# Performance work log

Hardware: AMD Instinct MI355X
Metric: run time of the kernel (lower is better)

## Reference

```python
import jax, jax.numpy as jnp
import numpy as np
from jax import lax

BN_EPS = 1e-5


def _conv(x, w):
    # stride-1, VALID conv; the torch 'locally connected' layer shares weights
    # across pixels, so it is exactly a standard conv2d.
    return lax.conv_general_dilated(
        x, w, window_strides=(1, 1), padding='VALID',
        dimension_numbers=('NCHW', 'OIHW', 'NCHW'))


def _batchnorm(x, gamma, beta):
    # training-mode BatchNorm2d: batch statistics over (N, H, W)
    mean = jnp.mean(x, axis=(0, 2, 3), keepdims=True)
    var = jnp.var(x, axis=(0, 2, 3), keepdims=True)
    xhat = (x - mean) * lax.rsqrt(var + BN_EPS)
    return xhat * gamma[None, :, None, None] + beta[None, :, None, None]


def setup_inputs() -> dict:
    key = jax.random.key(0)
    ks = jax.random.split(key, 6)
    B = 16384
    x = jax.random.normal(ks[0], (B, 256), dtype=jnp.float32)
    w1 = jax.random.normal(ks[1], (16, 1, 3, 3), dtype=jnp.float32)
    w2 = jax.random.normal(ks[2], (32, 16, 2, 2), dtype=jnp.float32)
    w3 = jax.random.normal(ks[3], (64, 32, 1, 1), dtype=jnp.float32)
    fan_in = 64 * 13 * 13
    bound = 1.0 / np.sqrt(fan_in)
    fc_w = jax.random.uniform(ks[4], (10, fan_in), minval=-bound, maxval=bound, dtype=jnp.float32)
    fc_b = jax.random.uniform(ks[5], (10,), minval=-bound, maxval=bound, dtype=jnp.float32)
    return {
        'x': x, 'w1': w1, 'w2': w2, 'w3': w3,
        'g1': jnp.ones((16,), jnp.float32), 'b1': jnp.zeros((16,), jnp.float32),
        'g2': jnp.ones((32,), jnp.float32), 'b2': jnp.zeros((32,), jnp.float32),
        'g3': jnp.ones((64,), jnp.float32), 'b3': jnp.zeros((64,), jnp.float32),
        'fc_w': fc_w, 'fc_b': fc_b,
    }


def reference(x, w1, w2, w3, g1, b1, g2, b2, g3, b3, fc_w, fc_b):
    h = x.reshape(-1, 1, 16, 16)                     # [B,1,16,16]
    h = jax.nn.relu(_batchnorm(_conv(h, w1), g1, b1))  # [B,16,14,14]
    h = jax.nn.relu(_batchnorm(_conv(h, w2), g2, b2))  # [B,32,13,13]
    h = jax.nn.relu(_batchnorm(_conv(h, w3), g3, b3))  # [B,64,13,13]
    h = h.reshape(h.shape[0], -1)                    # [B, 64*13*13]
    # dropout is identity in eval/deterministic mode
    return h @ fc_w.T + fc_b                         # [B,10]
```

## Files before the change

### kernel.cpp

```cpp
#include <hip/hip_runtime.h>


#define NPART 1024
#define P2_OFF 32768
#define ST_OFF 229376
#define ST1 ST_OFF
#define ST2 (ST_OFF + 32)
#define ST3 (ST_OFF + 96)
#define C2R_OFF 230400
#define C1R_OFF 231424
#define C2P_OFF 262144
#define A2G_BYTE 5242880ull
#define FCB_N (13 * 8192)
#define A1S 24
#define A1B 384
#define A3P 1048

typedef __attribute__((ext_vector_type(8))) short bf16x8;
typedef __attribute__((ext_vector_type(4))) float f32x4;
typedef __attribute__((ext_vector_type(4))) unsigned int u32x4;

__device__ __forceinline__ unsigned int f2bf(float f) {
  unsigned int u = __float_as_uint(f);
  return (u + 0x7fffu + ((u >> 16) & 1u)) >> 16;
}
__device__ __forceinline__ unsigned int pkbf(float a, float b) {
  unsigned ua = __float_as_uint(a) + 0x8000u;
  unsigned ub = __float_as_uint(b) + 0x8000u;
  return __builtin_amdgcn_perm(ub, ua, 0x07060302u);
}
__device__ __forceinline__ short cvtbf(float a) {
  return (short)((__float_as_uint(a) + 0x8000u) >> 16);
}
__device__ __forceinline__ bf16x8 mkfrag(uint2 a, uint2 b) {
  u32x4 u = {a.x, a.y, b.x, b.y};
  return __builtin_bit_cast(bf16x8, u);
}

__device__ __forceinline__ void conv1_mfma(
    const float* __restrict__ sxi,
    short* ph_buf,
    int r, int b, int q, bf16x8 a1f, f32x4 c1i)
{
  bf16x8 bf = {0, 0, 0, 0, 0, 0, 0, 0};
  unsigned* bu = (unsigned*)&bf;
  if (q == 0) {
    bu[0] = pkbf(sxi[r * 16 + b],           sxi[r * 16 + b + 1]);
    bu[1] = pkbf(sxi[r * 16 + b + 2],       sxi[(r + 1) * 16 + b]);
    bu[2] = pkbf(sxi[(r + 1) * 16 + b + 1], sxi[(r + 1) * 16 + b + 2]);
    bu[3] = pkbf(sxi[(r + 2) * 16 + b],     sxi[(r + 2) * 16 + b + 1]);
  } else if (q == 1) {
    bu[0] = pkbf(sxi[(r + 2) * 16 + b + 2], 0.f);
  }
  f32x4 acc = c1i;
  acc = __builtin_amdgcn_mfma_f32_16x16x32_bf16(a1f, bf, acc, 0, 0, 0);
  float v0 = acc[0] > 0.f ? acc[0] : 0.f;
  float v1 = acc[1] > 0.f ? acc[1] : 0.f;
  float v2 = acc[2] > 0.f ? acc[2] : 0.f;
  float v3 = acc[3] > 0.f ? acc[3] : 0.f;
  uint2 pk;
  pk.x = pkbf(v0, v1);
  pk.y = pkbf(v2, v3);
  *(uint2*)(ph_buf + (r & 1) * A1B + b * A1S + 4 * q) = pk;
}

__device__ __forceinline__ bf16x8 conv1_afrag(const float* w1, float rs1b,
                                              int b, int q) {
  bf16x8 v;
#pragma unroll
  for (int j = 0; j < 8; ++j) {
    int tap = 8 * q + j;
    v[j] = (tap < 9) ? (short)f2bf(w1[b * 9 + tap] * rs1b) : (short)0;
  }
  return v;
}

__global__ __launch_bounds__(256) void k1_xsyrk(
    const float* __restrict__ x, float* __restrict__ parts)
{
  __shared__ float sx[16 * 256];
  const int tid = threadIdx.x, w = tid >> 6, lane = tid & 63;
  const int b = lane & 15, q = lane >> 4;
  {
    const float4* xs = (const float4*)(x + (size_t)blockIdx.x * (16 * 256));
    float4* sd = (float4*)sx;
    for (int e = tid; e < 16 * 64; e += 256) sd[e] = xs[e];
  }
  __syncthreads();
  const int di = (b < 9) ? (b / 3) : 0;
  const int dj = (b < 9) ? (b - di * 3) : 0;
  const int h = q >> 1, jb = (q & 1) * 8;
  f32x4 acc = {0.f, 0.f, 0.f, 0.f};
#pragma unroll 1
  for (int t = 0; t < 4; ++t) {
    const float* sxi = sx + (w * 4 + t) * 256;
#pragma unroll 1
    for (int s = 0; s < 7; ++s) {
      bf16x8 af;
      unsigned* au = (unsigned*)&af;
      if (b < 9) {
        const float* srow = sxi + (2 * s + h + di) * 16 + dj;
#pragma unroll
        for (int cc = 0; cc < 4; ++cc) {
          float v0 = (jb + 2 * cc     < 14) ? srow[jb + 2 * cc]     : 0.f;
          float v1 = (jb + 2 * cc + 1 < 14) ? srow[jb + 2 * cc + 1] : 0.f;
          au[cc] = pkbf(v0, v1);
        }
      } else if (b == 9) {
#pragma unroll
        for (int cc = 0; cc < 4; ++cc) {
          unsigned lo = (jb + 2 * cc     < 14) ? 0x3F80u : 0u;
          unsigned hi = (jb + 2 * cc + 1 < 14) ? 0x3F800000u : 0u;
          au[cc] = lo | hi;
        }
      } else {
#pragma unroll
        for (int cc = 0; cc < 4; ++cc) au[cc] = 0u;
      }
      acc = __builtin_amdgcn_mfma_f32_16x16x32_bf16(af, af, acc, 0, 0, 0);
    }
  }
  __syncthreads();
  float* redc = sx;
#pragma unroll
  for (int rr = 0; rr < 4; ++rr)
    redc[w * 256 + (4 * q + rr) * 16 + b] = acc[rr];
  __syncthreads();
  parts[blockIdx.x * 256 + tid] =
      redc[tid] + redc[256 + tid] + redc[512 + tid] + redc[768 + tid];
}

__global__ __launch_bounds__(256) void k_stats1a(
    const float* __restrict__ parts, float* __restrict__ ws)
{
  const int e = blockIdx.x, tid = threadIdx.x;
  const int w = tid >> 6, lane = tid & 63;
  __shared__ float rs[4];
  float s = 0.f;
#pragma unroll 4
  for (int i = tid; i < 1024; i += 256) s += parts[i * 256 + e];
#pragma unroll
  for (int d = 1; d < 64; d <<= 1) s += __shfl_xor(s, d);
  if (lane == 0) rs[w] = s;
  __syncthreads();
  if (tid == 0) ws[C1R_OFF + e] = rs[0] + rs[1] + rs[2] + rs[3];
}

__global__ __launch_bounds__(64) void k_stats1b(
    const float* __restrict__ w1, const float* __restrict__ gamma,
    const float* __restrict__ beta, float* __restrict__ ws)
{
  const int c = threadIdx.x;
  if (c >= 16) return;
  const float* C = ws + C1R_OFF;
  float wr[9];
#pragma unroll
  for (int p = 0; p < 9; ++p) wr[p] = w1[c * 9 + p];
  float msum = 0.f;
#pragma unroll
  for (int p = 0; p < 9; ++p) msum += wr[p] * C[9 * 16 + p];
  float e2 = 0.f;
#pragma unroll
  for (int a = 0; a < 9; ++a)
#pragma unroll
    for (int bb = 0; bb < 9; ++bb)
      e2 += wr[a] * wr[bb] * C[a * 16 + bb];
  const float inv_n = 1.0f / (16384.0f * 196.0f);
  float mean = msum * inv_n;
  float var  = e2 * inv_n - mean * mean;
  float sv   = gamma[c] * rsqrtf(var + 1e-5f);
  ws[ST1 + c]      = sv;
  ws[ST1 + 16 + c] = beta[c] - mean * sv;
}

__global__ __launch_bounds__(256) void k_stats2(
    const float* __restrict__ gamma, const float* __restrict__ beta,
    float* __restrict__ ws, int nch, int part_off, int st_off, float inv_n)
{
  const int c = blockIdx.x, tid = threadIdx.x;
  const int w = tid >> 6, lane = tid & 63;
  __shared__ float rs[4], rq[4];
  float s = 0.f, q = 0.f;
#pragma unroll 4
  for (int i = tid; i < NPART; i += 256) {
    s += ws[part_off + i * 2 * nch + c];
    q += ws[part_off + i * 2 * nch + nch + c];
  }
#pragma unroll
  for (int d = 1; d < 64; d <<= 1) {
    s += __shfl_xor(s, d);
    q += __shfl_xor(q, d);
  }
  if (lane == 0) { rs[w] = s; rq[w] = q; }
  __syncthreads();
  if (tid == 0) {
    float st = rs[0] + rs[1] + rs[2] + rs[3];
    float qt = rq[0] + rq[1] + rq[2] + rq[3];
    float mean = st * inv_n;
    float var  = qt * inv_n - mean * mean;
    float sv   = gamma[c] * rsqrtf(var + 1e-5f);
    ws[st_off + c]       = sv;
    ws[st_off + nch + c] = beta[c] - mean * sv;
  }
}

__global__ __launch_bounds__(256) void k3_conv2_stats(
    const float* __restrict__ x, const float* __restrict__ w1,
    const float* __restrict__ w2, float* __restrict__ ws)
{
  __shared__ float sx_s[16 * 256 + 16];
  __shared__ alignas(16) short a1h[4 * 2 * A1B];
  __shared__ float redf[256];
  const int tid = threadIdx.x, w = tid >> 6, lane = tid & 63;
  const int b = lane & 15, q = lane >> 4;
  {
    const float4* xs = (const float4*)(x + (size_t)blockIdx.x * (16 * 256));
    float4* sd = (float4*)sx_s;
    for (int e = tid; e < 16 * 64; e += 256) sd[e] = xs[e];
    if (tid < 16) sx_s[16 * 256 + tid] = 0.f;
  }
  bf16x8 a1f = conv1_afrag(w1, ws[ST1 + b], b, q);
  f32x4 c1i;
#pragma unroll
  for (int r = 0; r < 4; ++r) c1i[r] = ws[ST1 + 16 + 4 * q + r];
  bf16x8 b2h[4];
#pragma unroll
  for (int ks = 0; ks < 2; ++ks)
#pragma unroll
    for (int nt = 0; nt < 2; ++nt) {
      bf16x8 vh;
#pragma unroll
      for (int j = 0; j < 8; ++j) {
        int kk = 8 * (q & 1) + j, dj = q >> 1;
        vh[j] = (short)f2bf(w2[(nt * 16 + b) * 64 + kk * 4 + ks * 2 + dj]);
      }
      b2h[ks * 2 + nt] = vh;
    }
  const float vb = (b < 13) ? 1.f : 0.f;
  const int colAr = (b + (q >> 1) < 15) ? (b + (q >> 1)) : 15;
  const int offAl = colAr * A1S + 8 * (q & 1);
  __syncthreads();

  float s2r[2][4] = {{0.f,0.f,0.f,0.f},{0.f,0.f,0.f,0.f}};
  float q2r[2][4] = {{0.f,0.f,0.f,0.f},{0.f,0.f,0.f,0.f}};
  short* ph = a1h + w * (2 * A1B);
#pragma unroll 1
  for (int t = 0; t < 4; ++t) {
    const float* sxi = sx_s + (w * 4 + t) * 256;
    conv1_mfma(sxi, ph, 0, b, q, a1f, c1i);
    __builtin_amdgcn_wave_barrier();
#pragma unroll 1
    for (int i = 0; i < 13; ++i) {
      conv1_mfma(sxi, ph, i + 1, b, q, a1f, c1i);
      __builtin_amdgcn_wave_barrier();
      bf16x8 ah0 = *(const bf16x8*)(ph + (i & 1) * A1B + offAl);
      bf16x8 ah1 = *(const bf16x8*)(ph + ((i + 1) & 1) * A1B + offAl);
      f32x4 acc2[2] = {{0.f,0.f,0.f,0.f},{0.f,0.f,0.f,0.f}};
#pragma unroll
      for (int nt = 0; nt < 2; ++nt) {
        acc2[nt] = __builtin_amdgcn_mfma_f32_16x16x32_bf16(b2h[nt], ah0, acc2[nt], 0, 0, 0);
        acc2[nt] = __builtin_amdgcn_mfma_f32_16x16x32_bf16(b2h[2 + nt], ah1, acc2[nt], 0, 0, 0);
      }
#pragma unroll
      for (int nt = 0; nt < 2; ++nt)
#pragma unroll
        for (int r = 0; r < 4; ++r) {
          float ym = acc2[nt][r] * vb;
          s2r[nt][r] += ym;
          q2r[nt][r] = fmaf(ym, acc2[nt][r], q2r[nt][r]);
        }
      __builtin_amdgcn_wave_barrier();
    }
  }
#pragma unroll
  for (int nt = 0; nt < 2; ++nt)
#pragma unroll
    for (int r = 0; r < 4; ++r) {
      float sv = s2r[nt][r], qv = q2r[nt][r];
      sv += __shfl_xor(sv, 1); sv += __shfl_xor(sv, 2);
      sv += __shfl_xor(sv, 4); sv += __shfl_xor(sv, 8);
      qv += __shfl_xor(qv, 1); qv += __shfl_xor(qv, 2);
      qv += __shfl_xor(qv, 4); qv += __shfl_xor(qv, 8);
      if (b == 0) {
        redf[w * 64 + nt * 16 + 4 * q + r]      = sv;
        redf[w * 64 + 32 + nt * 16 + 4 * q + r] = qv;
      }
    }
  __syncthreads();
  if (tid < 64)
    ws[P2_OFF + blockIdx.x * 64 + tid] =
        redf[tid] + redf[64 + tid] + redf[128 + tid] + redf[192 + tid];
}

__global__ __launch_bounds__(256) void k5_a2(
    const float* __restrict__ x, const float* __restrict__ w1,
    const float* __restrict__ w2, float* __restrict__ ws,
    short* __restrict__ a2g, float* __restrict__ parts)
{
  __shared__ float sx_s[16 * 256 + 16];
  __shared__ alignas(16) short a1h[4 * 2 * A1B];
  __shared__ float s2red[4 * 32];
  const int tid = threadIdx.x, w = tid >> 6, lane = tid & 63;
  const int b = lane & 15, q = lane >> 4;
  {
    const float4* xs = (const float4*)(x + (size_t)blockIdx.x * (16 * 256));
    float4* sd = (float4*)sx_s;
    for (int e = tid; e < 16 * 64; e += 256) sd[e] = xs[e];
    if (tid < 16) sx_s[16 * 256 + tid] = 0.f;
  }
  bf16x8 a1f = conv1_afrag(w1, ws[ST1 + b], b, q);
  f32x4 c1i;
#pragma unroll
  for (int r = 0; r < 4; ++r) c1i[r] = ws[ST1 + 16 + 4 * q + r];
  bf16x8 b2h[4];
#pragma unroll
  for (int ks = 0; ks < 2; ++ks)
#pragma unroll
    for (int nt = 0; nt < 2; ++nt) {
      float rs2b = ws[ST2 + nt * 16 + b];
      bf16x8 vh;
#pragma unroll
      for (int j = 0; j < 8; ++j) {
        int kk = 8 * (q & 1) + j, dj = q >> 1;
        vh[j] = (short)f2bf(w2[(nt * 16 + b) * 64 + kk * 4 + ks * 2 + dj] * rs2b);
      }
      b2h[ks * 2 + nt] = vh;
    }
  f32x4 c2i[2];
#pragma unroll
  for (int nt = 0; nt < 2; ++nt) {
    float t2b = ws[ST2 + 32 + nt * 16 + b];
#pragma unroll
    for (int r = 0; r < 4; ++r)
      c2i[nt][r] = (4 * q + r < 13) ? t2b : -1e30f;
  }
  const int colAr = (b + (q >> 1) < 15) ? (b + (q >> 1)) : 15;
  const int offAl = colAr * A1S + 8 * (q & 1);
  const u32x4 ou = {0x3F803F80u, 0x3F803F80u, 0x3F803F80u, 0x3F803F80u};
  const bf16x8 ones = __builtin_bit_cast(bf16x8, ou);
  __syncthreads();

  f32x4 accT0 = {0.f,0.f,0.f,0.f}, accT1 = {0.f,0.f,0.f,0.f},
        accT2 = {0.f,0.f,0.f,0.f};
  f32x4 accS0 = {0.f,0.f,0.f,0.f}, accS1 = {0.f,0.f,0.f,0.f};
  short* ph = a1h + w * (2 * A1B);
#pragma unroll 1
  for (int t = 0; t < 4; ++t) {
    const int img = blockIdx.x * 16 + w * 4 + t;
    const float* sxi = sx_s + (w * 4 + t) * 256;
    short* p0 = a2g + (size_t)img * 5408 + (size_t)(4 * q) * 32 + b;
    conv1_mfma(sxi, ph, 0, b, q, a1f, c1i);
    __builtin_amdgcn_wave_barrier();
    uint2 pkp[2];
#pragma unroll 1
    for (int i = 0; i < 13; ++i) {
      conv1_mfma(sxi, ph, i + 1, b, q, a1f, c1i);
      __builtin_amdgcn_wave_barrier();
      bf16x8 ah0 = *(const bf16x8*)(ph + (i & 1) * A1B + offAl);
      bf16x8 ah1 = *(const bf16x8*)(ph + ((i + 1) & 1) * A1B + offAl);
      uint2 pkc[2];
#pragma unroll
      for (int nt = 0; nt < 2; ++nt) {
        f32x4 acc2 = c2i[nt];
        acc2 = __builtin_amdgcn_mfma_f32_16x16x32_bf16(ah0, b2h[nt], acc2, 0, 0, 0);
        acc2 = __builtin_amdgcn_mfma_f32_16x16x32_bf16(ah1, b2h[2 + nt], acc2, 0, 0, 0);
        float v0 = acc2[0] > 0.f ? acc2[0] : 0.f;
        float v1 = acc2[1] > 0.f ? acc2[1] : 0.f;
        float v2 = acc2[2] > 0.f ? acc2[2] : 0.f;
        float v3 = acc2[3] > 0.f ? acc2[3] : 0.f;
        uint2 pk;
        pk.x = pkbf(v0, v1);
        pk.y = pkbf(v2, v3);
        short* pp = p0 + nt * 16;
        pp[0] = (short)pk.x;
        if (q < 3) {
          pp[32] = (short)(pk.x >> 16);
          pp[64] = (short)pk.y;
          pp[96] = (short)(pk.y >> 16);
        }
        pkc[nt] = pk;
      }
      p0 += 416;
      if (i & 1) {
        bf16x8 xf0 = mkfrag(pkp[0], pkc[0]);
        bf16x8 xf1 = mkfrag(pkp[1], pkc[1]);
        accT0 = __builtin_amdgcn_mfma_f32_16x16x32_bf16(xf0, xf0, accT0, 0, 0, 0);
        accT1 = __builtin_amdgcn_mfma_f32_16x16x32_bf16(xf0, xf1, accT1, 0, 0, 0);
        accT2 = __builtin_amdgcn_mfma_f32_16x16x32_bf16(xf1, xf1, accT2, 0, 0, 0);
        accS0 = __builtin_amdgcn_mfma_f32_16x16x32_bf16(ones, xf0, accS0, 0, 0, 0);
        accS1 = __builtin_amdgcn_mfma_f32_16x16x32_bf16(ones, xf1, accS1, 0, 0, 0);
      } else {
        pkp[0] = pkc[0];
        pkp[1] = pkc[1];
      }
      __builtin_amdgcn_wave_barrier();
    }
    {
      uint2 zz; zz.x = 0u; zz.y = 0u;
      bf16x8 xf0 = mkfrag(pkp[0], zz);
      bf16x8 xf1 = mkfrag(pkp[1], zz);
      accT0 = __builtin_amdgcn_mfma_f32_16x16x32_bf16(xf0, xf0, accT0, 0, 0, 0);
      accT1 = __builtin_amdgcn_mfma_f32_16x16x32_bf16(xf0, xf1, accT1, 0, 0, 0);
      accT2 = __builtin_amdgcn_mfma_f32_16x16x32_bf16(xf1, xf1, accT2, 0, 0, 0);
      accS0 = __builtin_amdgcn_mfma_f32_16x16x32_bf16(ones, xf0, accS0, 0, 0, 0);
      accS1 = __builtin_amdgcn_mfma_f32_16x16x32_bf16(ones, xf1, accS1, 0, 0, 0);
    }
  }
  if (q == 0) {
    s2red[w * 32 + b]      = accS0[0];
    s2red[w * 32 + 16 + b] = accS1[0];
  }
  float* redc = sx_s;
#pragma unroll
  for (int rr = 0; rr < 4; ++rr) {
    int m = 4 * q + rr;
    redc[w * 1024 + 0   + m * 16 + b] = accT0[rr];
    redc[w * 1024 + 256 + m * 16 + b] = accT1[rr];
    redc[w * 1024 + 512 + m * 16 + b] = accT2[rr];
  }
  __syncthreads();
  for (int e = tid; e < 768; e += 256)
    parts[blockIdx.x * 800 + e] =
        redc[e] + redc[1024 + e] + redc[2048 + e] + redc[3072 + e];
  if (tid < 32)
    parts[blockIdx.x * 800 + 768 + tid] =
        s2red[tid] + s2red[32 + tid] + s2red[64 + tid] + s2red[96 + tid];
}

__global__ __launch_bounds__(256) void k_statsC(
    const float* __restrict__ parts, float* __restrict__ ws)
{
  const int e = blockIdx.x, tid = threadIdx.x;
  const int w = tid >> 6, lane = tid & 63;
  __shared__ float rs[4];
  float s = 0.f;
#pragma unroll 4
  for (int i = tid; i < 1024; i += 256) s += parts[i * 800 + e];
#pragma unroll
  for (int d = 1; d < 64; d <<= 1) s += __shfl_xor(s, d);
  if (lane == 0) rs[w] = s;
  __syncthreads();
  if (tid == 0) ws[C2R_OFF + e] = rs[0] + rs[1] + rs[2] + rs[3];
}

__global__ __launch_bounds__(64) void k_stats3n(
    const float* __restrict__ w3, const float* __restrict__ gamma,
    const float* __restrict__ beta, float* __restrict__ ws)
{
  const int c3 = threadIdx.x;
  if (c3 >= 64) return;
  const float* C2R = ws + C2R_OFF;
  float wr[32];
#pragma unroll
  for (int k = 0; k < 32; ++k) wr[k] = w3[c3 * 32 + k];
  const float inv_n = 1.0f / (16384.0f * 169.0f);
  float msum = 0.f;
#pragma unroll
  for (int k = 0; k < 32; ++k) msum += wr[k] * C2R[768 + k];
  float e2 = 0.f;
  for (int a = 0; a < 16; ++a)
#pragma unroll
    for (int bb = 0; bb < 16; ++bb) {
      e2 += wr[a] * wr[bb] * C2R[a * 16 + bb];
      e2 += wr[16 + a] * wr[16 + bb] * C2R[512 + a * 16 + bb];
      e2 += 2.f * wr[a] * wr[16 + bb] * C2R[256 + a * 16 + bb];
    }
  float mean = msum * inv_n;
  float var  = e2 * inv_n - mean * mean;
  float sv   = gamma[c3] * rsqrtf(var + 1e-5f);
  ws[ST3 + c3]      = sv;
  ws[ST3 + 64 + c3] = beta[c3] - mean * sv;
}

__global__ __launch_bounds__(256) void k0_fcB(
    const float* __restrict__ fcw, unsigned int* __restrict__ fcB)
{
  int F = blockIdx.x * 256 + threadIdx.x;
  if (F >= FCB_N) return;
  int u = F & 3, q = (F >> 2) & 3, jj = (F >> 4) & 15;
  int mm = (F >> 8) & 31, i = F >> 13;
  int k0 = mm * 32 + q * 8 + u * 2;
  unsigned lo = 0, hi = 0;
  if (jj < 10) {
    int c0 = k0 >> 4, j0 = k0 & 15;
    if (j0 < 13) lo = f2bf(fcw[jj * 10816 + c0 * 169 + i * 13 + j0]);
    int c1 = (k0 + 1) >> 4, j1 = (k0 + 1) & 15;
    if (j1 < 13) hi = f2bf(fcw[jj * 10816 + c1 * 169 + i * 13 + j1]);
  }
  fcB[F] = lo | (hi << 16);
}

__global__ __launch_bounds__(256) void k7_fc(
    const short* __restrict__ a2g, const float* __restrict__ w3,
    const float* __restrict__ fcb, const float* __restrict__ ws,
    float* __restrict__ out)
{
  __shared__ alignas(16) short a3buf[16 * A3P];
  const int tid = threadIdx.x, w = tid >> 6, lane = tid & 63;
  const int b = lane & 15, q = lane >> 4;
  bf16x8 b3h[4];
  f32x4 c3i[4];
#pragma unroll
  for (int nt = 0; nt < 4; ++nt) {
    float s3 = ws[ST3 + nt * 16 + b];
    float t3 = ws[ST3 + 64 + nt * 16 + b];
    bf16x8 vh;
#pragma unroll
    for (int j = 0; j < 8; ++j)
      vh[j] = (short)f2bf(w3[(nt * 16 + b) * 32 + 8 * q + j] * s3);
    b3h[nt] = vh;
    c3i[nt][0] = t3;
#pragma unroll
    for (int r = 1; r < 4; ++r)
      c3i[nt][r] = (q < 3) ? t3 : -1e30f;
  }
  const bf16x8* fcB = (const bf16x8*)ws;
  f32x4 accF = {0.f, 0.f, 0.f, 0.f};
  const int pixc = (b < 12) ? b : 12;
  size_t ib[4];
#pragma unroll
  for (int t = 0; t < 4; ++t)
    ib[t] = (size_t)(blockIdx.x * 16 + w * 4 + t) * 5408;
  bf16x8 a2pre[4];
#pragma unroll
  for (int t = 0; t < 4; ++t)
    a2pre[t] = *(const bf16x8*)(a2g + ib[t] + pixc * 32 + 8 * q);

#pragma unroll 1
  for (int i = 0; i < 13; ++i) {
    bf16x8 a2cur[4];
#pragma unroll
    for (int t = 0; t < 4; ++t) a2cur[t] = a2pre[t];
    if (i < 12) {
#pragma unroll
      for (int t = 0; t < 4; ++t)
        a2pre[t] = *(const bf16x8*)(a2g + ib[t] +
                                    (size_t)((i + 1) * 13 + pixc) * 32 + 8 * q);
    }
#pragma unroll
    for (int t = 0; t < 4; ++t) {
      const int g = w * 4 + t;
#pragma unroll
      for (int nt = 0; nt < 4; ++nt) {
        f32x4 acc3 = c3i[nt];
        acc3 = __builtin_amdgcn_mfma_f32_16x16x32_bf16(a2cur[t], b3h[nt], acc3, 0, 0, 0);
        float v0 = acc3[0] > 0.f ? acc3[0] : 0.f;
        float v1 = acc3[1] > 0.f ? acc3[1] : 0.f;
        float v2 = acc3[2] > 0.f ? acc3[2] : 0.f;
        float v3 = acc3[3] > 0.f ? acc3[3] : 0.f;
        uint2 pk2;
        pk2.x = pkbf(v0, v1);
        pk2.y = pkbf(v2, v3);
        *(uint2*)(a3buf + g * A3P + (nt * 16 + b) * 16 + 4 * q) = pk2;
      }
    }
    __syncthreads();
#pragma unroll
    for (int mm = 0; mm < 8; ++mm) {
      bf16x8 af = *(const bf16x8*)(a3buf + b * A3P + w * 256 + mm * 32 + 8 * q);
      bf16x8 bw = fcB[((i * 32 + w * 8 + mm) * 16 + b) * 4 + q];
      accF = __builtin_amdgcn_mfma_f32_16x16x32_bf16(af, bw, accF, 0, 0, 0);
    }
    __syncthreads();
  }

  float* redf7 = (float*)a3buf;
#pragma unroll
  for (int r = 0; r < 4; ++r)
    redf7[w * 256 + (4 * q + r) * 16 + b] = accF[r];
  __syncthreads();
  if (tid < 160) {
    int img = tid / 10, jj = tid - img * 10;
    float s = redf7[img * 16 + jj] + redf7[256 + img * 16 + jj] +
              redf7[512 + img * 16 + jj] + redf7[768 + img * 16 + jj];
    out[(blockIdx.x * 16 + img) * 10 + jj] = s + fcb[jj];
  }
}

extern "C" void kernel_launch(void* const* d_in, const int* in_sizes, int n_in,
                              void* d_out, int out_size, void* d_ws, size_t ws_size,
                              hipStream_t stream) {
  (void)in_sizes; (void)n_in; (void)out_size; (void)ws_size;
  const float* x   = (const float*)d_in[0];
  const float* w1  = (const float*)d_in[1];
  const float* w2  = (const float*)d_in[2];
  const float* w3  = (const float*)d_in[3];
  const float* g1  = (const float*)d_in[4];
  const float* b1  = (const float*)d_in[5];
  const float* g2  = (const float*)d_in[6];
  const float* b2  = (const float*)d_in[7];
  const float* g3  = (const float*)d_in[8];
  const float* b3  = (const float*)d_in[9];
  const float* fcw = (const float*)d_in[10];
  const float* fcb = (const float*)d_in[11];
  float* out = (float*)d_out;
  float* ws  = (float*)d_ws;
  short* a2g = (short*)((char*)d_ws + A2G_BYTE);
  float* parts = ws + C2P_OFF;

  k1_xsyrk<<<1024, 256, 0, stream>>>(x, parts);
  k_stats1a<<<256, 256, 0, stream>>>(parts, ws);
  k_stats1b<<<1, 64, 0, stream>>>(w1, g1, b1, ws);
  k3_conv2_stats<<<1024, 256, 0, stream>>>(x, w1, w2, ws);
  k_stats2<<<32, 256, 0, stream>>>(g2, b2, ws, 32, P2_OFF, ST2,
                                   1.0f / (16384.0f * 169.0f));
  k5_a2<<<1024, 256, 0, stream>>>(x, w1, w2, ws, a2g, parts);
  k_statsC<<<800, 256, 0, stream>>>(parts, ws);
  k_stats3n<<<1, 64, 0, stream>>>(w3, g3, b3, ws);
  k0_fcB<<<FCB_N / 256, 256, 0, stream>>>(fcw, (unsigned int*)ws);
  k7_fc<<<1024, 256, 0, stream>>>(a2g, w3, fcb, ws, out);
}
```

Measured before the change: 279.5 us.

## Halve images per block and replace statsC reduction kernel with atomics

Each block in the stats and conv2 kernels now processes 8 images instead of 16, doubling the grid to 2048 blocks, and partial-sum buffers are sized for 2048 parts. The k_statsC reduction kernel is removed: k5_a2 combines wave partials in shared memory with a two-phase store/add and atomically adds its Gram-matrix and sum partials into the final workspace slots, which k_stats2 now zeroes. This aims to improve occupancy and latency hiding and to drop one kernel launch plus a partial-buffer round trip. In exchange it adds heavy float atomic contention on 800 addresses from 2048 blocks, and the summation order is no longer deterministic.

```diff
diff --git a/kernel.cpp b/kernel.cpp
--- a/kernel.cpp
+++ b/kernel.cpp
@@ -1,7 +1,7 @@
 #include <hip/hip_runtime.h>
 
 
-#define NPART 1024
+#define NPART 2048
 #define P2_OFF 32768
 #define ST_OFF 229376
 #define ST1 ST_OFF
@@ -29,9 +29,6 @@
   unsigned ub = __float_as_uint(b) + 0x8000u;
   return __builtin_amdgcn_perm(ub, ua, 0x07060302u);
 }
-__device__ __forceinline__ short cvtbf(float a) {
-  return (short)((__float_as_uint(a) + 0x8000u) >> 16);
-}
 __device__ __forceinline__ bf16x8 mkfrag(uint2 a, uint2 b) {
   u32x4 u = {a.x, a.y, b.x, b.y};
   return __builtin_bit_cast(bf16x8, u);
@@ -78,13 +75,13 @@
 __global__ __launch_bounds__(256) void k1_xsyrk(
     const float* __restrict__ x, float* __restrict__ parts)
 {
-  __shared__ float sx[16 * 256];
+  __shared__ float sx[8 * 256];
   const int tid = threadIdx.x, w = tid >> 6, lane = tid & 63;
   const int b = lane & 15, q = lane >> 4;
   {
-    const float4* xs = (const float4*)(x + (size_t)blockIdx.x * (16 * 256));
+    const float4* xs = (const float4*)(x + (size_t)blockIdx.x * (8 * 256));
     float4* sd = (float4*)sx;
-    for (int e = tid; e < 16 * 64; e += 256) sd[e] = xs[e];
+    for (int e = tid; e < 8 * 64; e += 256) sd[e] = xs[e];
   }
   __syncthreads();
   const int di = (b < 9) ? (b / 3) : 0;
@@ -92,8 +89,8 @@
   const int h = q >> 1, jb = (q & 1) * 8;
   f32x4 acc = {0.f, 0.f, 0.f, 0.f};
 #pragma unroll 1
-  for (int t = 0; t < 4; ++t) {
-    const float* sxi = sx + (w * 4 + t) * 256;
+  for (int t = 0; t < 2; ++t) {
+    const float* sxi = sx + (w * 2 + t) * 256;
 #pragma unroll 1
     for (int s = 0; s < 7; ++s) {
       bf16x8 af;
@@ -138,7 +135,7 @@
   __shared__ float rs[4];
   float s = 0.f;
 #pragma unroll 4
-  for (int i = tid; i < 1024; i += 256) s += parts[i * 256 + e];
+  for (int i = tid; i < 2048; i += 256) s += parts[i * 256 + e];
 #pragma unroll
   for (int d = 1; d < 64; d <<= 1) s += __shfl_xor(s, d);
   if (lane == 0) rs[w] = s;
@@ -179,6 +176,10 @@
 {
   const int c = blockIdx.x, tid = threadIdx.x;
   const int w = tid >> 6, lane = tid & 63;
+  {
+    int z = blockIdx.x * 256 + tid;
+    if (z < 800) ws[C2R_OFF + z] = 0.f;
+  }
   __shared__ float rs[4], rq[4];
   float s = 0.f, q = 0.f;
 #pragma unroll 4
@@ -208,16 +209,16 @@
     const float* __restrict__ x, const float* __restrict__ w1,
     const float* __restrict__ w2, float* __restrict__ ws)
 {
-  __shared__ float sx_s[16 * 256 + 16];
+  __shared__ float sx_s[8 * 256 + 16];
   __shared__ alignas(16) short a1h[4 * 2 * A1B];
   __shared__ float redf[256];
   const int tid = threadIdx.x, w = tid >> 6, lane = tid & 63;
   const int b = lane & 15, q = lane >> 4;
   {
-    const float4* xs = (const float4*)(x + (size_t)blockIdx.x * (16 * 256));
+    const float4* xs = (const float4*)(x + (size_t)blockIdx.x * (8 * 256));
     float4* sd = (float4*)sx_s;
-    for (int e = tid; e < 16 * 64; e += 256) sd[e] = xs[e];
-    if (tid < 16) sx_s[16 * 256 + tid] = 0.f;
+    for (int e = tid; e < 8 * 64; e += 256) sd[e] = xs[e];
+    if (tid < 16) sx_s[8 * 256 + tid] = 0.f;
   }
   bf16x8 a1f = conv1_afrag(w1, ws[ST1 + b], b, q);
   f32x4 c1i;
@@ -245,8 +246,8 @@
   float q2r[2][4] = {{0.f,0.f,0.f,0.f},{0.f,0.f,0.f,0.f}};
   short* ph = a1h + w * (2 * A1B);
 #pragma unroll 1
-  for (int t = 0; t < 4; ++t) {
-    const float* sxi = sx_s + (w * 4 + t) * 256;
+  for (int t = 0; t < 2; ++t) {
+    const float* sxi = sx_s + (w * 2 + t) * 256;
     conv1_mfma(sxi, ph, 0, b, q, a1f, c1i);
     __builtin_amdgcn_wave_barrier();
 #pragma unroll 1
@@ -295,18 +296,18 @@
 __global__ __launch_bounds__(256) void k5_a2(
     const float* __restrict__ x, const float* __restrict__ w1,
     const float* __restrict__ w2, float* __restrict__ ws,
-    short* __restrict__ a2g, float* __restrict__ parts)
-{
-  __shared__ float sx_s[16 * 256 + 16];
+    short* __restrict__ a2g)
+{
+  __shared__ float sx_s[2080];
   __shared__ alignas(16) short a1h[4 * 2 * A1B];
   __shared__ float s2red[4 * 32];
   const int tid = threadIdx.x, w = tid >> 6, lane = tid & 63;
   const int b = lane & 15, q = lane >> 4;
   {
-    const float4* xs = (const float4*)(x + (size_t)blockIdx.x * (16 * 256));
+    const float4* xs = (const float4*)(x + (size_t)blockIdx.x * (8 * 256));
     float4* sd = (float4*)sx_s;
-    for (int e = tid; e < 16 * 64; e += 256) sd[e] = xs[e];
-    if (tid < 16) sx_s[16 * 256 + tid] = 0.f;
+    for (int e = tid; e < 8 * 64; e += 256) sd[e] = xs[e];
+    if (tid < 16) sx_s[8 * 256 + tid] = 0.f;
   }
   bf16x8 a1f = conv1_afrag(w1, ws[ST1 + b], b, q);
   f32x4 c1i;
@@ -345,9 +346,9 @@
   f32x4 accS0 = {0.f,0.f,0.f,0.f}, accS1 = {0.f,0.f,0.f,0.f};
   short* ph = a1h + w * (2 * A1B);
 #pragma unroll 1
-  for (int t = 0; t < 4; ++t) {
-    const int img = blockIdx.x * 16 + w * 4 + t;
-    const float* sxi = sx_s + (w * 4 + t) * 256;
+  for (int t = 0; t < 2; ++t) {
+    const int img = blockIdx.x * 8 + w * 2 + t;
+    const float* sxi = sx_s + (w * 2 + t) * 256;
     short* p0 = a2g + (size_t)img * 5408 + (size_t)(4 * q) * 32 + b;
     conv1_mfma(sxi, ph, 0, b, q, a1f, c1i);
     __builtin_amdgcn_wave_barrier();
@@ -411,36 +412,33 @@
     s2red[w * 32 + 16 + b] = accS1[0];
   }
   float* redc = sx_s;
-#pragma unroll
-  for (int rr = 0; rr < 4; ++rr) {
-    int m = 4 * q + rr;
-    redc[w * 1024 + 0   + m * 16 + b] = accT0[rr];
-    redc[w * 1024 + 256 + m * 16 + b] = accT1[rr];
-    redc[w * 1024 + 512 + m * 16 + b] = accT2[rr];
+  __syncthreads();
+  if (w < 2) {
+#pragma unroll
+    for (int rr = 0; rr < 4; ++rr) {
+      int m = 4 * q + rr, base = w * 1024;
+      redc[base + 0   + m * 16 + b] = accT0[rr];
+      redc[base + 256 + m * 16 + b] = accT1[rr];
+      redc[base + 512 + m * 16 + b] = accT2[rr];
+    }
+  }
+  __syncthreads();
+  if (w >= 2) {
+#pragma unroll
+    for (int rr = 0; rr < 4; ++rr) {
+      int m = 4 * q + rr, base = (w - 2) * 1024;
+      redc[base + 0   + m * 16 + b] += accT0[rr];
+      redc[base + 256 + m * 16 + b] += accT1[rr];
+      redc[base + 512 + m * 16 + b] += accT2[rr];
+    }
   }
   __syncthreads();
   for (int e = tid; e < 768; e += 256)
-    parts[blockIdx.x * 800 + e] =
-        redc[e] + redc[1024 + e] + redc[2048 + e] + redc[3072 + e];
+    unsafeAtomicAdd(&ws[C2R_OFF + e], redc[e] + redc[1024 + e]);
   if (tid < 32)
-    parts[blockIdx.x * 800 + 768 + tid] =
-        s2red[tid] + s2red[32 + tid] + s2red[64 + tid] + s2red[96 + tid];
-}
-
-__global__ __launch_bounds__(256) void k_statsC(
-    const float* __restrict__ parts, float* __restrict__ ws)
-{
-  const int e = blockIdx.x, tid = threadIdx.x;
-  const int w = tid >> 6, lane = tid & 63;
-  __shared__ float rs[4];
-  float s = 0.f;
-#pragma unroll 4
-  for (int i = tid; i < 1024; i += 256) s += parts[i * 800 + e];
-#pragma unroll
-  for (int d = 1; d < 64; d <<= 1) s += __shfl_xor(s, d);
-  if (lane == 0) rs[w] = s;
-  __syncthreads();
-  if (tid == 0) ws[C2R_OFF + e] = rs[0] + rs[1] + rs[2] + rs[3];
+    unsafeAtomicAdd(&ws[C2R_OFF + 768 + tid],
+                    s2red[tid] + s2red[32 + tid] + s2red[64 + tid] +
+                    s2red[96 + tid]);
 }
 
 __global__ __launch_bounds__(64) void k_stats3n(
@@ -598,14 +596,13 @@
   short* a2g = (short*)((char*)d_ws + A2G_BYTE);
   float* parts = ws + C2P_OFF;
 
-  k1_xsyrk<<<1024, 256, 0, stream>>>(x, parts);
+  k1_xsyrk<<<2048, 256, 0, stream>>>(x, parts);
   k_stats1a<<<256, 256, 0, stream>>>(parts, ws);
   k_stats1b<<<1, 64, 0, stream>>>(w1, g1, b1, ws);
-  k3_conv2_stats<<<1024, 256, 0, stream>>>(x, w1, w2, ws);
+  k3_conv2_stats<<<2048, 256, 0, stream>>>(x, w1, w2, ws);
   k_stats2<<<32, 256, 0, stream>>>(g2, b2, ws, 32, P2_OFF, ST2,
                                    1.0f / (16384.0f * 169.0f));
-  k5_a2<<<1024, 256, 0, stream>>>(x, w1, w2, ws, a2g, parts);
-  k_statsC<<<800, 256, 0, stream>>>(parts, ws);
+  k5_a2<<<2048, 256, 0, stream>>>(x, w1, w2, ws, a2g);
   k_stats3n<<<1, 64, 0, stream>>>(w3, g3, b3, ws);
   k0_fcB<<<FCB_N / 256, 256, 0, stream>>>(fcw, (unsigned int*)ws);
   k7_fc<<<1024, 256, 0, stream>>>(a2g, w3, fcb, ws, out);
```

New measurement: 299.4 us. 1.07x slower.

## Chain conv3 MFMA output directly into FC MFMA registers, dropping LDS staging

Applied to the files above, without the earlier changes.

The final conv3+FC kernel now swaps the MFMA operand order so the conv3 result lands in a register layout that can be packed straight into the A operand of the FC MFMA. This removes the shared-memory round trip and both per-row barriers. Work is split by pixel ranges across the four waves, with 16 images per block. The FC weight pre-layout kernel is rewritten to match the new per-pixel, channel-pair fragment order, and the padded pixel columns are dropped. In exchange, each wave's loads are strided per image, and each iteration depends on a serial MFMA chain.

```diff
diff --git a/kernel.cpp b/kernel.cpp
--- a/kernel.cpp
+++ b/kernel.cpp
@@ -11,10 +11,9 @@
 #define C1R_OFF 231424
 #define C2P_OFF 262144
 #define A2G_BYTE 5242880ull
-#define FCB_N (13 * 8192)
+#define FCB_N 86528
 #define A1S 24
 #define A1B 384
-#define A3P 1048
 
 typedef __attribute__((ext_vector_type(8))) short bf16x8;
 typedef __attribute__((ext_vector_type(4))) float f32x4;
@@ -28,9 +27,6 @@
   unsigned ua = __float_as_uint(a) + 0x8000u;
   unsigned ub = __float_as_uint(b) + 0x8000u;
   return __builtin_amdgcn_perm(ub, ua, 0x07060302u);
-}
-__device__ __forceinline__ short cvtbf(float a) {
-  return (short)((__float_as_uint(a) + 0x8000u) >> 16);
 }
 __device__ __forceinline__ bf16x8 mkfrag(uint2 a, uint2 b) {
   u32x4 u = {a.x, a.y, b.x, b.y};
@@ -475,19 +471,16 @@
 __global__ __launch_bounds__(256) void k0_fcB(
     const float* __restrict__ fcw, unsigned int* __restrict__ fcB)
 {
-  int F = blockIdx.x * 256 + threadIdx.x;
-  if (F >= FCB_N) return;
-  int u = F & 3, q = (F >> 2) & 3, jj = (F >> 4) & 15;
-  int mm = (F >> 8) & 31, i = F >> 13;
-  int k0 = mm * 32 + q * 8 + u * 2;
+  int f = blockIdx.x * 256 + threadIdx.x;
+  int u = f & 3, lane = (f >> 2) & 63, h = (f >> 8) & 1, p = f >> 9;
+  int b = lane & 15, q = lane >> 4;
   unsigned lo = 0, hi = 0;
-  if (jj < 10) {
-    int c0 = k0 >> 4, j0 = k0 & 15;
-    if (j0 < 13) lo = f2bf(fcw[jj * 10816 + c0 * 169 + i * 13 + j0]);
-    int c1 = (k0 + 1) >> 4, j1 = (k0 + 1) & 15;
-    if (j1 < 13) hi = f2bf(fcw[jj * 10816 + c1 * 169 + i * 13 + j1]);
-  }
-  fcB[F] = lo | (hi << 16);
+  if (b < 10) {
+    int c30 = h * 32 + (u >> 1) * 16 + 4 * q + 2 * (u & 1);
+    lo = f2bf(fcw[b * 10816 + c30 * 169 + p]);
+    hi = f2bf(fcw[b * 10816 + (c30 + 1) * 169 + p]);
+  }
+  fcB[f] = lo | (hi << 16);
 }
 
 __global__ __launch_bounds__(256) void k7_fc(
@@ -495,7 +488,7 @@
     const float* __restrict__ fcb, const float* __restrict__ ws,
     float* __restrict__ out)
 {
-  __shared__ alignas(16) short a3buf[16 * A3P];
+  __shared__ float redf7[1024];
   const int tid = threadIdx.x, w = tid >> 6, lane = tid & 63;
   const int b = lane & 15, q = lane >> 4;
   bf16x8 b3h[4];
@@ -503,71 +496,48 @@
 #pragma unroll
   for (int nt = 0; nt < 4; ++nt) {
     float s3 = ws[ST3 + nt * 16 + b];
-    float t3 = ws[ST3 + 64 + nt * 16 + b];
     bf16x8 vh;
 #pragma unroll
     for (int j = 0; j < 8; ++j)
       vh[j] = (short)f2bf(w3[(nt * 16 + b) * 32 + 8 * q + j] * s3);
     b3h[nt] = vh;
-    c3i[nt][0] = t3;
-#pragma unroll
-    for (int r = 1; r < 4; ++r)
-      c3i[nt][r] = (q < 3) ? t3 : -1e30f;
+#pragma unroll
+    for (int r = 0; r < 4; ++r)
+      c3i[nt][r] = ws[ST3 + 64 + nt * 16 + 4 * q + r];
   }
   const bf16x8* fcB = (const bf16x8*)ws;
-  f32x4 accF = {0.f, 0.f, 0.f, 0.f};
-  const int pixc = (b < 12) ? b : 12;
-  size_t ib[4];
-#pragma unroll
-  for (int t = 0; t < 4; ++t)
-    ib[t] = (size_t)(blockIdx.x * 16 + w * 4 + t) * 5408;
-  bf16x8 a2pre[4];
-#pragma unroll
-  for (int t = 0; t < 4; ++t)
-    a2pre[t] = *(const bf16x8*)(a2g + ib[t] + pixc * 32 + 8 * q);
-
-#pragma unroll 1
-  for (int i = 0; i < 13; ++i) {
-    bf16x8 a2cur[4];
-#pragma unroll
-    for (int t = 0; t < 4; ++t) a2cur[t] = a2pre[t];
-    if (i < 12) {
-#pragma unroll
-      for (int t = 0; t < 4; ++t)
-        a2pre[t] = *(const bf16x8*)(a2g + ib[t] +
-                                    (size_t)((i + 1) * 13 + pixc) * 32 + 8 * q);
-    }
-#pragma unroll
-    for (int t = 0; t < 4; ++t) {
-      const int g = w * 4 + t;
-#pragma unroll
-      for (int nt = 0; nt < 4; ++nt) {
-        f32x4 acc3 = c3i[nt];
-        acc3 = __builtin_amdgcn_mfma_f32_16x16x32_bf16(a2cur[t], b3h[nt], acc3, 0, 0, 0);
-        float v0 = acc3[0] > 0.f ? acc3[0] : 0.f;
-        float v1 = acc3[1] > 0.f ? acc3[1] : 0.f;
-        float v2 = acc3[2] > 0.f ? acc3[2] : 0.f;
-        float v3 = acc3[3] > 0.f ? acc3[3] : 0.f;
-        uint2 pk2;
-        pk2.x = pkbf(v0, v1);
-        pk2.y = pkbf(v2, v3);
-        *(uint2*)(a3buf + g * A3P + (nt * 16 + b) * 16 + 4 * q) = pk2;
-      }
-    }
-    __syncthreads();
-#pragma unroll
-    for (int mm = 0; mm < 8; ++mm) {
-      bf16x8 af = *(const bf16x8*)(a3buf + b * A3P + w * 256 + mm * 32 + 8 * q);
-      bf16x8 bw = fcB[((i * 32 + w * 8 + mm) * 16 + b) * 4 + q];
-      accF = __builtin_amdgcn_mfma_f32_16x16x32_bf16(af, bw, accF, 0, 0, 0);
-    }
-    __syncthreads();
-  }
-
-  float* redf7 = (float*)a3buf;
+  const short* abase = a2g + (size_t)(blockIdx.x * 16 + b) * 5408 + 8 * q;
+  const int p0 = (w * 169) >> 2, p1 = ((w + 1) * 169) >> 2;
+  f32x4 aF0 = {0.f, 0.f, 0.f, 0.f}, aF1 = {0.f, 0.f, 0.f, 0.f};
+  bf16x8 vpre = *(const bf16x8*)(abase + p0 * 32);
+  bf16x8 bw0 = fcB[(p0 * 2 + 0) * 64 + lane];
+  bf16x8 bw1 = fcB[(p0 * 2 + 1) * 64 + lane];
+#pragma unroll 1
+  for (int p = p0; p < p1; ++p) {
+    bf16x8 vc = vpre, f0 = bw0, f1 = bw1;
+    if (p + 1 < p1) {
+      vpre = *(const bf16x8*)(abase + (p + 1) * 32);
+      bw0 = fcB[((p + 1) * 2 + 0) * 64 + lane];
+      bw1 = fcB[((p + 1) * 2 + 1) * 64 + lane];
+    }
+    uint2 pkc[4];
+#pragma unroll
+    for (int nt = 0; nt < 4; ++nt) {
+      f32x4 acc3 = c3i[nt];
+      acc3 = __builtin_amdgcn_mfma_f32_16x16x32_bf16(b3h[nt], vc, acc3, 0, 0, 0);
+      float v0 = acc3[0] > 0.f ? acc3[0] : 0.f;
+      float v1 = acc3[1] > 0.f ? acc3[1] : 0.f;
+      float v2 = acc3[2] > 0.f ? acc3[2] : 0.f;
+      float v3 = acc3[3] > 0.f ? acc3[3] : 0.f;
+      pkc[nt].x = pkbf(v0, v1);
+      pkc[nt].y = pkbf(v2, v3);
+    }
+    aF0 = __builtin_amdgcn_mfma_f32_16x16x32_bf16(mkfrag(pkc[0], pkc[1]), f0, aF0, 0, 0, 0);
+    aF1 = __builtin_amdgcn_mfma_f32_16x16x32_bf16(mkfrag(pkc[2], pkc[3]), f1, aF1, 0, 0, 0);
+  }
 #pragma unroll
   for (int r = 0; r < 4; ++r)
-    redf7[w * 256 + (4 * q + r) * 16 + b] = accF[r];
+    redf7[w * 256 + (4 * q + r) * 16 + b] = aF0[r] + aF1[r];
   __syncthreads();
   if (tid < 160) {
     int img = tid / 10, jj = tid - img * 10;
```

After: 259.1 us. -7.3%, faster.
